# Kernel optimization log

Hardware: AMD Instinct MI355X
Metric: run time of the kernel (lower is better)

Reference implementation:

```python
import jax, jax.numpy as jnp
import numpy as np

R, C, N, E, H, F, ED, G, L = 1, 4, 50000, 200000, 128, 128, 16, 64, 2


def setup_inputs() -> dict:
    key = jax.random.key(0)
    ks = jax.random.split(key, 16)
    s = 0.05
    return {
        "x": jax.random.normal(ks[0], (R * C * N, H), jnp.float32),
        "batch": jnp.sort(jax.random.randint(ks[1], (N,), 0, G)),
        "edge_index": jax.random.randint(ks[2], (2, E), 0, N),
        "edge_attr": jax.random.normal(ks[3], (1, 1, E, ED), jnp.float32),
        "node_mask": jax.random.uniform(ks[4], (R, C, N, 1), jnp.float32),
        "edge_mask": jax.random.uniform(ks[5], (R, C, E, 1), jnp.float32),
        "W_be": jax.random.normal(ks[6], (ED, H), jnp.float32) * s,
        "b_be": jnp.zeros((H,), jnp.float32),
        "eps": jnp.zeros((L,), jnp.float32),
        "W1": jax.random.normal(ks[7], (L, H, H), jnp.float32) * s,
        "b1": jnp.zeros((L, H), jnp.float32),
        "W2": jax.random.normal(ks[8], (L, H, H), jnp.float32) * s,
        "b2": jnp.zeros((L, H), jnp.float32),
        "Wm1": jax.random.normal(ks[9], (H, H), jnp.float32) * s,
        "bm1": jnp.zeros((H,), jnp.float32),
        "Wm2": jax.random.normal(ks[10], (H, F), jnp.float32) * s,
        "bm2": jnp.zeros((F,), jnp.float32),
    }


def reference(x, batch, edge_index, edge_attr, node_mask, edge_mask,
              W_be, b_be, eps, W1, b1, W2, b2, Wm1, bm1, Wm2, bm2):
    gelu = lambda v: jax.nn.gelu(v, approximate=False)  # torch F.gelu default is erf
    src, dst = edge_index[0], edge_index[1]
    # bond encoder, shared across conv layers: (1,1,E,H)
    ee = edge_attr @ W_be + b_be
    for l in range(L):
        ux = x.reshape(R, C, N, H)
        # gather + add + GELU + edge-weight multiply: (R,C,E,H)
        msg = gelu(ux[:, :, src, :] + ee) * edge_mask
        # scatter_sum over edges into destination nodes
        agg = jnp.zeros_like(ux).at[:, :, dst, :].add(msg)
        h = (1.0 + eps[l]) * x + agg.reshape(x.shape)
        # conv MLP: Linear -> GELU -> Linear, then outer GELU (norm=Identity, dropout=0)
        h = gelu(h @ W1[l] + b1[l]) @ W2[l] + b2[l]
        x = gelu(h)
    # final node MLP (PyG MLP, norm=None): Linear -> GELU -> Linear
    x = gelu(x @ Wm1 + bm1) @ Wm2 + bm2  # (R*C*N, F)
    x4 = x.reshape(R, C, N, F)
    # masked mean-pool per (repeat, centroid, graph)
    num = jnp.zeros((R, C, G, F), x.dtype).at[:, :, batch, :].add(x4 * node_mask)
    den = jnp.zeros((R, C, G, 1), x.dtype).at[:, :, batch, :].add(node_mask) + 1e-7
    pooled = (num / den).transpose(0, 2, 1, 3).reshape(-1, F)  # (R*G*C, F)
    return pooled
```

## Files before the change

### kernel.cpp

```cpp
#include <hip/hip_runtime.h>
#include <math.h>

#define NN 50000
#define EN 200000
#define CC 4
#define HH 128
#define GG 64
#define LDSA 136
#define LDSF 132

typedef __attribute__((ext_vector_type(8))) short bs8;
typedef __attribute__((ext_vector_type(4))) float f32x4;

__device__ __forceinline__ unsigned short f2bf(float f) {
  unsigned int u = __float_as_uint(f);
  u += 0x7FFFu + ((u >> 16) & 1u);
  return (unsigned short)(u >> 16);
}
__device__ __forceinline__ float bf2f(unsigned short h) {
  return __uint_as_float(((unsigned int)h) << 16);
}
__device__ __forceinline__ float gelu_f(float x) {
  float z = fabsf(x) * 0.7071067811865476f;
  float t = __builtin_amdgcn_rcpf(fmaf(0.3275911f, z, 1.0f));
  float poly = t * fmaf(t, fmaf(t, fmaf(t, fmaf(t, 1.061405429f, -1.453152027f),
                                        1.421413741f), -0.284496736f), 0.254829592f);
  float e = fmaf(-poly, __expf(-z * z), 1.0f);
  return 0.5f * x * (1.0f + copysignf(e, x));
}
__device__ __forceinline__ float gelu2_f(float x) {
  float z = fabsf(x) * 0.7071067811865476f;
  float t = __builtin_amdgcn_rcpf(fmaf(0.3275911f, z, 1.0f));
  float poly = t * fmaf(t, fmaf(t, fmaf(t, fmaf(t, 1.061405429f, -1.453152027f),
                                        1.421413741f), -0.284496736f), 0.254829592f);
  float e = fmaf(-poly, __expf(-z * z), 1.0f);
  return x * (1.0f + copysignf(e, x));
}

__global__ __launch_bounds__(256) void count_kernel(const int* __restrict__ dst,
                                                    int* __restrict__ counts) {
  int e = blockIdx.x * 256 + threadIdx.x;
  if (e < EN) atomicAdd(&counts[dst[e]], 1);
}

__global__ __launch_bounds__(256) void block_sum_kernel(const int* __restrict__ counts,
                                                        int* __restrict__ bsums) {
  int tid = threadIdx.x;
  int i = blockIdx.x * 256 + tid;
  int v = (i < NN) ? counts[i] : 0;
#pragma unroll
  for (int d = 1; d < 64; d <<= 1) v += __shfl_xor(v, d);
  __shared__ int ws4[4];
  if ((tid & 63) == 0) ws4[tid >> 6] = v;
  __syncthreads();
  if (tid == 0) bsums[blockIdx.x] = ws4[0] + ws4[1] + ws4[2] + ws4[3];
}

__global__ __launch_bounds__(256) void bsum_scan_kernel(const int* __restrict__ bsums,
                                                        int* __restrict__ boffs, int nb) {
  int tid = threadIdx.x, lane = tid & 63, wv = tid >> 6;
  int v = (tid < nb) ? bsums[tid] : 0;
  int s = v;
#pragma unroll
  for (int d = 1; d < 64; d <<= 1) { int t = __shfl_up(s, d); if (lane >= d) s += t; }
  __shared__ int wsum[4];
  if (lane == 63) wsum[wv] = s;
  __syncthreads();
  int pre = 0;
  for (int j = 0; j < wv; ++j) pre += wsum[j];
  if (tid < nb) boffs[tid] = pre + s - v;
}

__global__ __launch_bounds__(256) void block_scan_kernel(const int* __restrict__ counts,
                                                         const int* __restrict__ boffs,
                                                         int* __restrict__ offsets,
                                                         int* __restrict__ cursor) {
  int tid = threadIdx.x, lane = tid & 63, wv = tid >> 6;
  int i = blockIdx.x * 256 + tid;
  int v = (i < NN) ? counts[i] : 0;
  int s = v;
#pragma unroll
  for (int d = 1; d < 64; d <<= 1) { int t = __shfl_up(s, d); if (lane >= d) s += t; }
  __shared__ int wsum[4];
  if (lane == 63) wsum[wv] = s;
  __syncthreads();
  int pre = boffs[blockIdx.x];
  for (int j = 0; j < wv; ++j) pre += wsum[j];
  if (i < NN) { int e = pre + s - v; offsets[i] = e; cursor[i] = e; }
  if (i == 0) offsets[NN] = EN;
}

__global__ __launch_bounds__(256) void fill_kernel(const int* __restrict__ dst,
                                                   int* __restrict__ cursor,
                                                   int* __restrict__ csr_e) {
  int e = blockIdx.x * 256 + threadIdx.x;
  if (e < EN) {
    int pos = atomicAdd(&cursor[dst[e]], 1);
    csr_e[pos] = e;
  }
}

__global__ __launch_bounds__(256) void prep_w_kernel(const float* __restrict__ W1,
                                                     const float* __restrict__ W2,
                                                     const float* __restrict__ Wm1,
                                                     const float* __restrict__ Wm2,
                                                     unsigned short* __restrict__ wts) {
  int m = blockIdx.x >> 6;
  int idx = (blockIdx.x & 63) * 256 + threadIdx.x;
  const float* src = (m == 0) ? W1 : (m == 1) ? W1 + 16384 : (m == 2) ? W2
                     : (m == 3) ? W2 + 16384 : (m == 4) ? Wm1 : Wm2;
  unsigned short* dhi = wts + m * 32768;
  unsigned short* dlo = dhi + 16384;
  int n = idx >> 7, k = idx & 127;
  float v = src[k * HH + n];
  unsigned short hi = f2bf(v);
  dhi[n * HH + k] = hi;
  dlo[n * HH + k] = f2bf(v - bf2f(hi));
}

__global__ __launch_bounds__(256) void ee_kernel(const float* __restrict__ eattr,
                                                 const float* __restrict__ Wbe,
                                                 const float* __restrict__ bbe,
                                                 float* __restrict__ ee) {
  __shared__ float Ws[16 * HH];
  __shared__ float Ea[16 * 16];
  int tid = threadIdx.x;
  int e0 = blockIdx.x * 16;
#pragma unroll
  for (int i = 0; i < 8; ++i) Ws[tid + i * 256] = Wbe[tid + i * 256];
  Ea[tid] = eattr[(size_t)e0 * 16 + tid];
  __syncthreads();
  int h = tid & 127, half = tid >> 7;
  float bb = bbe[h];
#pragma unroll
  for (int j = 0; j < 8; ++j) {
    int el = j * 2 + half;
    float acc = bb;
#pragma unroll
    for (int d = 0; d < 16; ++d) acc += Ea[el * 16 + d] * Ws[d * HH + h];
    ee[(size_t)(e0 + el) * HH + h] = acc;
  }
}

__global__ __launch_bounds__(256) void agg_kernel(const float* __restrict__ x,
                                                  const float* __restrict__ ee,
                                                  const float* __restrict__ emask,
                                                  const int* __restrict__ src,
                                                  const int* __restrict__ off,
                                                  const int* __restrict__ csr_e,
                                                  const float* __restrict__ epsp, int layer,
                                                  float* __restrict__ hout) {
  int wv = threadIdx.x >> 6, lane = threadIdx.x & 63;
  int v = blockIdx.x * 4 + wv;
  int c2 = lane * 2;
  float2 acc[CC];
#pragma unroll
  for (int c = 0; c < CC; ++c) { acc[c].x = 0.f; acc[c].y = 0.f; }
  int beg = off[v], end = off[v + 1];

  float2 eeC; float2 xC[CC]; float emC[CC];
  int eN = 0, sN = 0;
  eeC.x = 0.f; eeC.y = 0.f;
#pragma unroll
  for (int c = 0; c < CC; ++c) { xC[c].x = 0.f; xC[c].y = 0.f; emC[c] = 0.f; }

  if (beg < end) {
    int e0 = csr_e[beg];
    int s0 = src[e0];
    eeC = *(const float2*)(ee + (size_t)e0 * HH + c2);
#pragma unroll
    for (int c = 0; c < CC; ++c) {
      xC[c] = *(const float2*)(x + ((size_t)c * NN + s0) * HH + c2);
      emC[c] = 0.5f * emask[(size_t)c * EN + e0];
    }
    if (beg + 1 < end) { eN = csr_e[beg + 1]; sN = src[eN]; }
  }

  for (int t = beg; t < end; ++t) {
    float2 eeB; float2 xB[CC]; float emB[CC];
    int eNN = 0, sNN = 0;
    if (t + 1 < end) {
      eeB = *(const float2*)(ee + (size_t)eN * HH + c2);
#pragma unroll
      for (int c = 0; c < CC; ++c) {
        xB[c] = *(const float2*)(x + ((size_t)c * NN + sN) * HH + c2);
        emB[c] = 0.5f * emask[(size_t)c * EN + eN];
      }
      if (t + 2 < end) { eNN = csr_e[t + 2]; sNN = src[eNN]; }
    } else {
      eeB.x = 0.f; eeB.y = 0.f;
#pragma unroll
      for (int c = 0; c < CC; ++c) { xB[c].x = 0.f; xB[c].y = 0.f; emB[c] = 0.f; }
    }
#pragma unroll
    for (int c = 0; c < CC; ++c) {
      acc[c].x += gelu2_f(xC[c].x + eeC.x) * emC[c];
      acc[c].y += gelu2_f(xC[c].y + eeC.y) * emC[c];
    }
    eeC = eeB;
#pragma unroll
    for (int c = 0; c < CC; ++c) { xC[c] = xB[c]; emC[c] = emB[c]; }
    eN = eNN; sN = sNN;
  }

  float ep = 1.0f + epsp[layer];
#pragma unroll
  for (int c = 0; c < CC; ++c) {
    float2 xs = *(const float2*)(x + ((size_t)c * NN + v) * HH + c2);
    float2 o;
    o.x = fmaf(ep, xs.x, acc[c].x);
    o.y = fmaf(ep, xs.y, acc[c].y);
    *(float2*)(hout + ((size_t)c * NN + v) * HH + c2) = o;
  }
}

__global__ __launch_bounds__(256, 2) void mlp_kernel(
    const float* __restrict__ in,
    const unsigned short* __restrict__ w1hi, const unsigned short* __restrict__ w1lo,
    const float* __restrict__ b1,
    const unsigned short* __restrict__ w2hi, const unsigned short* __restrict__ w2lo,
    const float* __restrict__ b2,
    float* __restrict__ out) {
  __shared__ __align__(16) unsigned short AB[2 * 64 * HH];
  unsigned short* Ahi = AB;
  unsigned short* Alo = AB + 64 * HH;
  int tid = threadIdx.x;
  int row0 = blockIdx.x * 64;
  int lane = tid & 63, wq = tid >> 6;
  int ln = lane & 15, quad = lane >> 4;

  bs8 b1h[4][2], b1l[4][2];
#pragma unroll
  for (int ks = 0; ks < 4; ++ks)
#pragma unroll
    for (int nt = 0; nt < 2; ++nt) {
      int wrow = ((wq * 2 + nt) * 16 + ln) * HH + ks * 32 + quad * 8;
      b1h[ks][nt] = *(const bs8*)(w1hi + wrow);
      b1l[ks][nt] = *(const bs8*)(w1lo + wrow);
    }

#pragma unroll
  for (int i = 0; i < 4; ++i) {
    int idx = tid + i * 256;
    int r = idx >> 4, blk = idx & 15;
    const float* p = in + (size_t)(row0 + r) * HH + blk * 8;
    float4 v0 = *(const float4*)p;
    float4 v1 = *(const float4*)(p + 4);
    bs8 h, l;
    h[0] = f2bf(v0.x); h[1] = f2bf(v0.y); h[2] = f2bf(v0.z); h[3] = f2bf(v0.w);
    h[4] = f2bf(v1.x); h[5] = f2bf(v1.y); h[6] = f2bf(v1.z); h[7] = f2bf(v1.w);
    l[0] = f2bf(v0.x - bf2f(h[0])); l[1] = f2bf(v0.y - bf2f(h[1]));
    l[2] = f2bf(v0.z - bf2f(h[2])); l[3] = f2bf(v0.w - bf2f(h[3]));
    l[4] = f2bf(v1.x - bf2f(h[4])); l[5] = f2bf(v1.y - bf2f(h[5]));
    l[6] = f2bf(v1.z - bf2f(h[6])); l[7] = f2bf(v1.w - bf2f(h[7]));
    int sb = blk ^ (r & 15);
    *(bs8*)(Ahi + r * HH + sb * 8) = h;
    *(bs8*)(Alo + r * HH + sb * 8) = l;
  }
  __syncthreads();

  f32x4 acc[4][2];
#pragma unroll
  for (int mt = 0; mt < 4; ++mt)
#pragma unroll
    for (int nt = 0; nt < 2; ++nt)
#pragma unroll
      for (int r = 0; r < 4; ++r) acc[mt][nt][r] = 0.f;
#pragma unroll
  for (int ks = 0; ks < 4; ++ks) {
    bs8 ah[4], al[4];
    int sb = ((ks * 4 + quad) ^ ln) * 8;
#pragma unroll
    for (int mt = 0; mt < 4; ++mt) {
      ah[mt] = *(const bs8*)(Ahi + (mt * 16 + ln) * HH + sb);
      al[mt] = *(const bs8*)(Alo + (mt * 16 + ln) * HH + sb);
    }
#pragma unroll
    for (int nt = 0; nt < 2; ++nt)
#pragma unroll
      for (int mt = 0; mt < 4; ++mt) {
        acc[mt][nt] = __builtin_amdgcn_mfma_f32_16x16x32_bf16(al[mt], b1h[ks][nt], acc[mt][nt], 0, 0, 0);
        acc[mt][nt] = __builtin_amdgcn_mfma_f32_16x16x32_bf16(ah[mt], b1l[ks][nt], acc[mt][nt], 0, 0, 0);
        acc[mt][nt] = __builtin_amdgcn_mfma_f32_16x16x32_bf16(ah[mt], b1h[ks][nt], acc[mt][nt], 0, 0, 0);
      }
  }
  __syncthreads();

  bs8 b2h[4][2], b2l[4][2];
#pragma unroll
  for (int ks = 0; ks < 4; ++ks)
#pragma unroll
    for (int nt = 0; nt < 2; ++nt) {
      int wrow = ((wq * 2 + nt) * 16 + ln) * HH + ks * 32 + quad * 8;
      b2h[ks][nt] = *(const bs8*)(w2hi + wrow);
      b2l[ks][nt] = *(const bs8*)(w2lo + wrow);
    }

#pragma unroll
  for (int nt = 0; nt < 2; ++nt) {
    int col = (wq * 2 + nt) * 16 + ln;
    int cb = col >> 3, co = col & 7;
    float bb = b1[col];
#pragma unroll
    for (int mt = 0; mt < 4; ++mt)
#pragma unroll
      for (int r = 0; r < 4; ++r) {
        float tv = gelu_f(acc[mt][nt][r] + bb);
        unsigned short th = f2bf(tv);
        int rr = mt * 16 + quad * 4 + r;
        int sof = rr * HH + (cb ^ (rr & 15)) * 8 + co;
        Ahi[sof] = th;
        Alo[sof] = f2bf(tv - bf2f(th));
      }
  }
  __syncthreads();

#pragma unroll
  for (int mt = 0; mt < 4; ++mt)
#pragma unroll
    for (int nt = 0; nt < 2; ++nt)
#pragma unroll
      for (int r = 0; r < 4; ++r) acc[mt][nt][r] = 0.f;
#pragma unroll
  for (int ks = 0; ks < 4; ++ks) {
    bs8 ah[4], al[4];
    int sb = ((ks * 4 + quad) ^ ln) * 8;
#pragma unroll
    for (int mt = 0; mt < 4; ++mt) {
      ah[mt] = *(const bs8*)(Ahi + (mt * 16 + ln) * HH + sb);
      al[mt] = *(const bs8*)(Alo + (mt * 16 + ln) * HH + sb);
    }
#pragma unroll
    for (int nt = 0; nt < 2; ++nt)
#pragma unroll
      for (int mt = 0; mt < 4; ++mt) {
        acc[mt][nt] = __builtin_amdgcn_mfma_f32_16x16x32_bf16(al[mt], b2h[ks][nt], acc[mt][nt], 0, 0, 0);
        acc[mt][nt] = __builtin_amdgcn_mfma_f32_16x16x32_bf16(ah[mt], b2l[ks][nt], acc[mt][nt], 0, 0, 0);
        acc[mt][nt] = __builtin_amdgcn_mfma_f32_16x16x32_bf16(ah[mt], b2h[ks][nt], acc[mt][nt], 0, 0, 0);
      }
  }
#pragma unroll
  for (int nt = 0; nt < 2; ++nt) {
    int col = (wq * 2 + nt) * 16 + ln;
    float bb = b2[col];
#pragma unroll
    for (int mt = 0; mt < 4; ++mt)
#pragma unroll
      for (int r = 0; r < 4; ++r) {
        float o = gelu_f(acc[mt][nt][r] + bb);
        out[(size_t)(row0 + mt * 16 + quad * 4 + r) * HH + col] = o;
      }
  }
}

__global__ __launch_bounds__(256, 2) void mlp_pool_kernel(
    const float* __restrict__ in,
    const unsigned short* __restrict__ w1hi, const unsigned short* __restrict__ w1lo,
    const float* __restrict__ b1,
    const unsigned short* __restrict__ w2hi, const unsigned short* __restrict__ w2lo,
    const float* __restrict__ b2,
    const float* __restrict__ nmask, const int* __restrict__ batch,
    float* __restrict__ num) {
  __shared__ __align__(16) unsigned short AB[128 * LDSA];
  __shared__ int kk[64];
  unsigned short* Ahi = AB;
  unsigned short* Alo = AB + 64 * LDSA;
  int tid = threadIdx.x;
  int row0 = blockIdx.x * 64;
  int lane = tid & 63, wq = tid >> 6;
  int ln = lane & 15, quad = lane >> 4;

  bs8 b1h[4][2], b1l[4][2];
#pragma unroll
  for (int ks = 0; ks < 4; ++ks)
#pragma unroll
    for (int nt = 0; nt < 2; ++nt) {
      int wrow = ((wq * 2 + nt) * 16 + ln) * HH + ks * 32 + quad * 8;
      b1h[ks][nt] = *(const bs8*)(w1hi + wrow);
      b1l[ks][nt] = *(const bs8*)(w1lo + wrow);
    }
#pragma unroll
  for (int i = 0; i < 8; ++i) {
    int idx = tid + i * 256;
    int r = idx >> 5, cc4 = idx & 31;
    float4 vv = *(const float4*)(in + (size_t)(row0 + r) * HH + cc4 * 4);
    unsigned short h0 = f2bf(vv.x), h1 = f2bf(vv.y), h2 = f2bf(vv.z), h3 = f2bf(vv.w);
    ushort4 hv; hv.x = h0; hv.y = h1; hv.z = h2; hv.w = h3;
    ushort4 lv;
    lv.x = f2bf(vv.x - bf2f(h0)); lv.y = f2bf(vv.y - bf2f(h1));
    lv.z = f2bf(vv.z - bf2f(h2)); lv.w = f2bf(vv.w - bf2f(h3));
    *(ushort4*)(Ahi + r * LDSA + cc4 * 4) = hv;
    *(ushort4*)(Alo + r * LDSA + cc4 * 4) = lv;
  }
  if (tid < 64) {
    int gr = row0 + tid;
    int c = gr / NN;
    int n = gr - c * NN;
    kk[tid] = (c << 6) | batch[n];
  }
  __syncthreads();

  f32x4 acc[4][2];
#pragma unroll
  for (int mt = 0; mt < 4; ++mt)
#pragma unroll
    for (int nt = 0; nt < 2; ++nt)
#pragma unroll
      for (int r = 0; r < 4; ++r) acc[mt][nt][r] = 0.f;
#pragma unroll
  for (int ks = 0; ks < 4; ++ks) {
    bs8 ah[4], al[4];
#pragma unroll
    for (int mt = 0; mt < 4; ++mt) {
      ah[mt] = *(const bs8*)(Ahi + (mt * 16 + ln) * LDSA + ks * 32 + quad * 8);
      al[mt] = *(const bs8*)(Alo + (mt * 16 + ln) * LDSA + ks * 32 + quad * 8);
    }
#pragma unroll
    for (int nt = 0; nt < 2; ++nt)
#pragma unroll
      for (int mt = 0; mt < 4; ++mt) {
        acc[mt][nt] = __builtin_amdgcn_mfma_f32_16x16x32_bf16(al[mt], b1h[ks][nt], acc[mt][nt], 0, 0, 0);
        acc[mt][nt] = __builtin_amdgcn_mfma_f32_16x16x32_bf16(ah[mt], b1l[ks][nt], acc[mt][nt], 0, 0, 0);
        acc[mt][nt] = __builtin_amdgcn_mfma_f32_16x16x32_bf16(ah[mt], b1h[ks][nt], acc[mt][nt], 0, 0, 0);
      }
  }
  __syncthreads();

  bs8 b2h[4][2], b2l[4][2];
#pragma unroll
  for (int ks = 0; ks < 4; ++ks)
#pragma unroll
    for (int nt = 0; nt < 2; ++nt) {
      int wrow = ((wq * 2 + nt) * 16 + ln) * HH + ks * 32 + quad * 8;
      b2h[ks][nt] = *(const bs8*)(w2hi + wrow);
      b2l[ks][nt] = *(const bs8*)(w2lo + wrow);
    }
#pragma unroll
  for (int nt = 0; nt < 2; ++nt) {
    int col = (wq * 2 + nt) * 16 + ln;
    float bb = b1[col];
#pragma unroll
    for (int mt = 0; mt < 4; ++mt)
#pragma unroll
      for (int r = 0; r < 4; ++r) {
        float tv = gelu_f(acc[mt][nt][r] + bb);
        unsigned short th = f2bf(tv);
        int rr = mt * 16 + quad * 4 + r;
        Ahi[rr * LDSA + col] = th;
        Alo[rr * LDSA + col] = f2bf(tv - bf2f(th));
      }
  }
  __syncthreads();

#pragma unroll
  for (int mt = 0; mt < 4; ++mt)
#pragma unroll
    for (int nt = 0; nt < 2; ++nt)
#pragma unroll
      for (int r = 0; r < 4; ++r) acc[mt][nt][r] = 0.f;
#pragma unroll
  for (int ks = 0; ks < 4; ++ks) {
    bs8 ah[4], al[4];
#pragma unroll
    for (int mt = 0; mt < 4; ++mt) {
      ah[mt] = *(const bs8*)(Ahi + (mt * 16 + ln) * LDSA + ks * 32 + quad * 8);
      al[mt] = *(const bs8*)(Alo + (mt * 16 + ln) * LDSA + ks * 32 + quad * 8);
    }
#pragma unroll
    for (int nt = 0; nt < 2; ++nt)
#pragma unroll
      for (int mt = 0; mt < 4; ++mt) {
        acc[mt][nt] = __builtin_amdgcn_mfma_f32_16x16x32_bf16(al[mt], b2h[ks][nt], acc[mt][nt], 0, 0, 0);
        acc[mt][nt] = __builtin_amdgcn_mfma_f32_16x16x32_bf16(ah[mt], b2l[ks][nt], acc[mt][nt], 0, 0, 0);
        acc[mt][nt] = __builtin_amdgcn_mfma_f32_16x16x32_bf16(ah[mt], b2h[ks][nt], acc[mt][nt], 0, 0, 0);
      }
  }
  __syncthreads();
  float* Tf = (float*)AB;
#pragma unroll
  for (int nt = 0; nt < 2; ++nt) {
    int col = (wq * 2 + nt) * 16 + ln;
    float bb = b2[col];
#pragma unroll
    for (int mt = 0; mt < 4; ++mt)
#pragma unroll
      for (int r = 0; r < 4; ++r) {
        int rl = mt * 16 + quad * 4 + r;
        int gr = row0 + rl;
        Tf[rl * LDSF + col] = (acc[mt][nt][r] + bb) * nmask[gr];
      }
  }
  __syncthreads();
  if (tid < 128) {
    int col = tid;
    float a2 = 0.f;
    int cur = kk[0];
    for (int r = 0; r < 64; ++r) {
      int k2 = kk[r];
      if (k2 != cur) {
        atomicAdd(&num[((size_t)(cur & 63) * CC + (cur >> 6)) * HH + col], a2);
        a2 = 0.f;
        cur = k2;
      }
      a2 += Tf[r * LDSF + col];
    }
    atomicAdd(&num[((size_t)(cur & 63) * CC + (cur >> 6)) * HH + col], a2);
  }
}

__global__ __launch_bounds__(256) void pool_finalize_kernel(const float* __restrict__ num,
                                                            const int* __restrict__ batch,
                                                            const float* __restrict__ nmask,
                                                            float* __restrict__ outp) {
  int g = blockIdx.x >> 2, c = blockIdx.x & 3;
  int lo = 0, hi = NN;
  while (lo < hi) { int m = (lo + hi) >> 1; if (batch[m] < g) lo = m + 1; else hi = m; }
  int start = lo;
  hi = NN;
  while (lo < hi) { int m = (lo + hi) >> 1; if (batch[m] < g + 1) lo = m + 1; else hi = m; }
  int end = lo;
  int tid = threadIdx.x;
  float d = 0.f;
  for (int n = start + tid; n < end; n += 256) d += nmask[c * NN + n];
#pragma unroll
  for (int k = 1; k < 64; k <<= 1) d += __shfl_xor(d, k);
  __shared__ float ws4[4];
  if ((tid & 63) == 0) ws4[tid >> 6] = d;
  __syncthreads();
  float den = ws4[0] + ws4[1] + ws4[2] + ws4[3] + 1e-7f;
  if (tid < 128) {
    int idx = blockIdx.x * 128 + tid;
    outp[idx] = num[idx] / den;
  }
}

extern "C" void kernel_launch(void* const* d_in, const int* in_sizes, int n_in,
                              void* d_out, int out_size, void* d_ws, size_t ws_size,
                              hipStream_t stream) {
  const float* x_in  = (const float*)d_in[0];
  const int*   batch = (const int*)d_in[1];
  const int*   eidx  = (const int*)d_in[2];
  const float* eattr = (const float*)d_in[3];
  const float* nmask = (const float*)d_in[4];
  const float* emask = (const float*)d_in[5];
  const float* Wbe   = (const float*)d_in[6];
  const float* bbe   = (const float*)d_in[7];
  const float* epsp  = (const float*)d_in[8];
  const float* W1    = (const float*)d_in[9];
  const float* b1    = (const float*)d_in[10];
  const float* W2    = (const float*)d_in[11];
  const float* b2    = (const float*)d_in[12];
  const float* Wm1   = (const float*)d_in[13];
  const float* bm1   = (const float*)d_in[14];
  const float* Wm2   = (const float*)d_in[15];
  const float* bm2   = (const float*)d_in[16];
  float* outp = (float*)d_out;

  const int* srcp = eidx;
  const int* dstp = eidx + EN;

  char* ws = (char*)d_ws;
  float* ee   = (float*)(ws);
  float* hbuf = (float*)(ws + 102400000);
  float* xbuf = (float*)(ws + 204800000);
  int* counts  = (int*)(ws + 307200000);
  int* offsets = counts + NN;
  int* cursor  = offsets + NN + 1;
  int* csr_e   = cursor + NN;
  unsigned short* wts = (unsigned short*)(ws + 307200000 + 1400016);
  int* bsums = (int*)ws;
  int* boffs = (int*)(ws + 1024);
  float* num = (float*)ws;

  const int NB = (NN + 255) / 256;

  hipMemsetAsync(counts, 0, NN * sizeof(int), stream);
  count_kernel<<<(EN + 255) / 256, 256, 0, stream>>>(dstp, counts);
  block_sum_kernel<<<NB, 256, 0, stream>>>(counts, bsums);
  bsum_scan_kernel<<<1, 256, 0, stream>>>(bsums, boffs, NB);
  block_scan_kernel<<<NB, 256, 0, stream>>>(counts, boffs, offsets, cursor);
  fill_kernel<<<(EN + 255) / 256, 256, 0, stream>>>(dstp, cursor, csr_e);

  prep_w_kernel<<<384, 256, 0, stream>>>(W1, W2, Wm1, Wm2, wts);

  ee_kernel<<<EN / 16, 256, 0, stream>>>(eattr, Wbe, bbe, ee);

  agg_kernel<<<NN / 4, 256, 0, stream>>>(x_in, ee, emask, srcp, offsets, csr_e, epsp, 0, hbuf);
  mlp_kernel<<<(CC * NN) / 64, 256, 0, stream>>>(hbuf, wts + 0, wts + 16384, b1,
                                                 wts + 65536, wts + 81920, b2, xbuf);
  agg_kernel<<<NN / 4, 256, 0, stream>>>(xbuf, ee, emask, srcp, offsets, csr_e, epsp, 1, hbuf);
  mlp_kernel<<<(CC * NN) / 64, 256, 0, stream>>>(hbuf, wts + 32768, wts + 49152, b1 + 128,
                                                 wts + 98304, wts + 114688, b2 + 128, xbuf);
  hipMemsetAsync(num, 0, 131072, stream);
  mlp_pool_kernel<<<(CC * NN) / 64, 256, 0, stream>>>(xbuf, wts + 131072, wts + 147456, bm1,
                                                      wts + 163840, wts + 180224, bm2,
                                                      nmask, batch, num);
  pool_finalize_kernel<<<GG * CC, 256, 0, stream>>>(num, batch, nmask, outp);
}
```

Baseline: 714.1 us.

## Pack edge src and masks into CSR order; use nontemporal streaming loads/stores

The CSR fill kernel now writes each edge's id and source index together, plus its four per-centroid edge masks as a float4, in destination-sorted order. The aggregation kernel then reads these contiguously instead of chasing csr_e→src and making four scattered emask loads per edge. The h buffer is now written with nontemporal stores and read back in the MLP kernels with nontemporal loads, to reduce cache pollution. The cost is a larger fill kernel and extra workspace for the packed arrays.

```diff
diff --git a/kernel.cpp b/kernel.cpp
--- a/kernel.cpp
+++ b/kernel.cpp
@@ -11,6 +11,7 @@
 
 typedef __attribute__((ext_vector_type(8))) short bs8;
 typedef __attribute__((ext_vector_type(4))) float f32x4;
+typedef __attribute__((ext_vector_type(2))) float f32x2;
 
 __device__ __forceinline__ unsigned short f2bf(float f) {
   unsigned int u = __float_as_uint(f);
@@ -91,12 +92,21 @@
 }
 
 __global__ __launch_bounds__(256) void fill_kernel(const int* __restrict__ dst,
+                                                   const int* __restrict__ src,
+                                                   const float* __restrict__ emask,
                                                    int* __restrict__ cursor,
-                                                   int* __restrict__ csr_e) {
+                                                   int2* __restrict__ csr_es,
+                                                   float4* __restrict__ emask_s) {
   int e = blockIdx.x * 256 + threadIdx.x;
   if (e < EN) {
+    int s = src[e];
+    float m0 = emask[e];
+    float m1 = emask[EN + e];
+    float m2 = emask[2 * EN + e];
+    float m3 = emask[3 * EN + e];
     int pos = atomicAdd(&cursor[dst[e]], 1);
-    csr_e[pos] = e;
+    csr_es[pos] = make_int2(e, s);
+    emask_s[pos] = make_float4(m0, m1, m2, m3);
   }
 }
 
@@ -144,10 +154,9 @@
 
 __global__ __launch_bounds__(256) void agg_kernel(const float* __restrict__ x,
                                                   const float* __restrict__ ee,
-                                                  const float* __restrict__ emask,
-                                                  const int* __restrict__ src,
                                                   const int* __restrict__ off,
-                                                  const int* __restrict__ csr_e,
+                                                  const int2* __restrict__ csr_es,
+                                                  const float4* __restrict__ emask_s,
                                                   const float* __restrict__ epsp, int layer,
                                                   float* __restrict__ hout) {
   int wv = threadIdx.x >> 6, lane = threadIdx.x & 63;
@@ -159,34 +168,33 @@
   int beg = off[v], end = off[v + 1];
 
   float2 eeC; float2 xC[CC]; float emC[CC];
-  int eN = 0, sN = 0;
+  int2 esN = make_int2(0, 0);
   eeC.x = 0.f; eeC.y = 0.f;
 #pragma unroll
   for (int c = 0; c < CC; ++c) { xC[c].x = 0.f; xC[c].y = 0.f; emC[c] = 0.f; }
 
   if (beg < end) {
-    int e0 = csr_e[beg];
-    int s0 = src[e0];
-    eeC = *(const float2*)(ee + (size_t)e0 * HH + c2);
-#pragma unroll
-    for (int c = 0; c < CC; ++c) {
-      xC[c] = *(const float2*)(x + ((size_t)c * NN + s0) * HH + c2);
-      emC[c] = 0.5f * emask[(size_t)c * EN + e0];
-    }
-    if (beg + 1 < end) { eN = csr_e[beg + 1]; sN = src[eN]; }
+    int2 es0 = csr_es[beg];
+    eeC = *(const float2*)(ee + (size_t)es0.x * HH + c2);
+#pragma unroll
+    for (int c = 0; c < CC; ++c)
+      xC[c] = *(const float2*)(x + ((size_t)c * NN + es0.y) * HH + c2);
+    float4 m = emask_s[beg];
+    emC[0] = 0.5f * m.x; emC[1] = 0.5f * m.y; emC[2] = 0.5f * m.z; emC[3] = 0.5f * m.w;
+    if (beg + 1 < end) esN = csr_es[beg + 1];
   }
 
   for (int t = beg; t < end; ++t) {
     float2 eeB; float2 xB[CC]; float emB[CC];
-    int eNN = 0, sNN = 0;
+    int2 esNN = make_int2(0, 0);
     if (t + 1 < end) {
-      eeB = *(const float2*)(ee + (size_t)eN * HH + c2);
-#pragma unroll
-      for (int c = 0; c < CC; ++c) {
-        xB[c] = *(const float2*)(x + ((size_t)c * NN + sN) * HH + c2);
-        emB[c] = 0.5f * emask[(size_t)c * EN + eN];
-      }
-      if (t + 2 < end) { eNN = csr_e[t + 2]; sNN = src[eNN]; }
+      eeB = *(const float2*)(ee + (size_t)esN.x * HH + c2);
+#pragma unroll
+      for (int c = 0; c < CC; ++c)
+        xB[c] = *(const float2*)(x + ((size_t)c * NN + esN.y) * HH + c2);
+      float4 m = emask_s[t + 1];
+      emB[0] = 0.5f * m.x; emB[1] = 0.5f * m.y; emB[2] = 0.5f * m.z; emB[3] = 0.5f * m.w;
+      if (t + 2 < end) esNN = csr_es[t + 2];
     } else {
       eeB.x = 0.f; eeB.y = 0.f;
 #pragma unroll
@@ -200,17 +208,17 @@
     eeC = eeB;
 #pragma unroll
     for (int c = 0; c < CC; ++c) { xC[c] = xB[c]; emC[c] = emB[c]; }
-    eN = eNN; sN = sNN;
+    esN = esNN;
   }
 
   float ep = 1.0f + epsp[layer];
 #pragma unroll
   for (int c = 0; c < CC; ++c) {
     float2 xs = *(const float2*)(x + ((size_t)c * NN + v) * HH + c2);
-    float2 o;
-    o.x = fmaf(ep, xs.x, acc[c].x);
-    o.y = fmaf(ep, xs.y, acc[c].y);
-    *(float2*)(hout + ((size_t)c * NN + v) * HH + c2) = o;
+    f32x2 o;
+    o[0] = fmaf(ep, xs.x, acc[c].x);
+    o[1] = fmaf(ep, xs.y, acc[c].y);
+    __builtin_nontemporal_store(o, (f32x2*)(hout + ((size_t)c * NN + v) * HH + c2));
   }
 }
 
@@ -244,15 +252,15 @@
     int idx = tid + i * 256;
     int r = idx >> 4, blk = idx & 15;
     const float* p = in + (size_t)(row0 + r) * HH + blk * 8;
-    float4 v0 = *(const float4*)p;
-    float4 v1 = *(const float4*)(p + 4);
+    f32x4 v0 = __builtin_nontemporal_load((const f32x4*)p);
+    f32x4 v1 = __builtin_nontemporal_load((const f32x4*)(p + 4));
     bs8 h, l;
-    h[0] = f2bf(v0.x); h[1] = f2bf(v0.y); h[2] = f2bf(v0.z); h[3] = f2bf(v0.w);
-    h[4] = f2bf(v1.x); h[5] = f2bf(v1.y); h[6] = f2bf(v1.z); h[7] = f2bf(v1.w);
-    l[0] = f2bf(v0.x - bf2f(h[0])); l[1] = f2bf(v0.y - bf2f(h[1]));
-    l[2] = f2bf(v0.z - bf2f(h[2])); l[3] = f2bf(v0.w - bf2f(h[3]));
-    l[4] = f2bf(v1.x - bf2f(h[4])); l[5] = f2bf(v1.y - bf2f(h[5]));
-    l[6] = f2bf(v1.z - bf2f(h[6])); l[7] = f2bf(v1.w - bf2f(h[7]));
+    h[0] = f2bf(v0[0]); h[1] = f2bf(v0[1]); h[2] = f2bf(v0[2]); h[3] = f2bf(v0[3]);
+    h[4] = f2bf(v1[0]); h[5] = f2bf(v1[1]); h[6] = f2bf(v1[2]); h[7] = f2bf(v1[3]);
+    l[0] = f2bf(v0[0] - bf2f(h[0])); l[1] = f2bf(v0[1] - bf2f(h[1]));
+    l[2] = f2bf(v0[2] - bf2f(h[2])); l[3] = f2bf(v0[3] - bf2f(h[3]));
+    l[4] = f2bf(v1[0] - bf2f(h[4])); l[5] = f2bf(v1[1] - bf2f(h[5]));
+    l[6] = f2bf(v1[2] - bf2f(h[6])); l[7] = f2bf(v1[3] - bf2f(h[7]));
     int sb = blk ^ (r & 15);
     *(bs8*)(Ahi + r * HH + sb * 8) = h;
     *(bs8*)(Alo + r * HH + sb * 8) = l;
@@ -383,12 +391,13 @@
   for (int i = 0; i < 8; ++i) {
     int idx = tid + i * 256;
     int r = idx >> 5, cc4 = idx & 31;
-    float4 vv = *(const float4*)(in + (size_t)(row0 + r) * HH + cc4 * 4);
-    unsigned short h0 = f2bf(vv.x), h1 = f2bf(vv.y), h2 = f2bf(vv.z), h3 = f2bf(vv.w);
+    f32x4 vv = __builtin_nontemporal_load(
+        (const f32x4*)(in + (size_t)(row0 + r) * HH + cc4 * 4));
+    unsigned short h0 = f2bf(vv[0]), h1 = f2bf(vv[1]), h2 = f2bf(vv[2]), h3 = f2bf(vv[3]);
     ushort4 hv; hv.x = h0; hv.y = h1; hv.z = h2; hv.w = h3;
     ushort4 lv;
-    lv.x = f2bf(vv.x - bf2f(h0)); lv.y = f2bf(vv.y - bf2f(h1));
-    lv.z = f2bf(vv.z - bf2f(h2)); lv.w = f2bf(vv.w - bf2f(h3));
+    lv.x = f2bf(vv[0] - bf2f(h0)); lv.y = f2bf(vv[1] - bf2f(h1));
+    lv.z = f2bf(vv[2] - bf2f(h2)); lv.w = f2bf(vv[3] - bf2f(h3));
     *(ushort4*)(Ahi + r * LDSA + cc4 * 4) = hv;
     *(ushort4*)(Alo + r * LDSA + cc4 * 4) = lv;
   }
@@ -564,10 +573,11 @@
   float* hbuf = (float*)(ws + 102400000);
   float* xbuf = (float*)(ws + 204800000);
   int* counts  = (int*)(ws + 307200000);
-  int* offsets = counts + NN;
-  int* cursor  = offsets + NN + 1;
-  int* csr_e   = cursor + NN;
-  unsigned short* wts = (unsigned short*)(ws + 307200000 + 1400016);
+  int* offsets = (int*)(ws + 307400000);
+  int* cursor  = (int*)(ws + 307600008);
+  int2* csr_es = (int2*)(ws + 307800016);
+  float4* emask_s = (float4*)(ws + 309400016);
+  unsigned short* wts = (unsigned short*)(ws + 312600016);
   int* bsums = (int*)ws;
   int* boffs = (int*)(ws + 1024);
   float* num = (float*)ws;
@@ -579,16 +589,16 @@
   block_sum_kernel<<<NB, 256, 0, stream>>>(counts, bsums);
   bsum_scan_kernel<<<1, 256, 0, stream>>>(bsums, boffs, NB);
   block_scan_kernel<<<NB, 256, 0, stream>>>(counts, boffs, offsets, cursor);
-  fill_kernel<<<(EN + 255) / 256, 256, 0, stream>>>(dstp, cursor, csr_e);
+  fill_kernel<<<(EN + 255) / 256, 256, 0, stream>>>(dstp, srcp, emask, cursor, csr_es, emask_s);
 
   prep_w_kernel<<<384, 256, 0, stream>>>(W1, W2, Wm1, Wm2, wts);
 
   ee_kernel<<<EN / 16, 256, 0, stream>>>(eattr, Wbe, bbe, ee);
 
-  agg_kernel<<<NN / 4, 256, 0, stream>>>(x_in, ee, emask, srcp, offsets, csr_e, epsp, 0, hbuf);
+  agg_kernel<<<NN / 4, 256, 0, stream>>>(x_in, ee, offsets, csr_es, emask_s, epsp, 0, hbuf);
   mlp_kernel<<<(CC * NN) / 64, 256, 0, stream>>>(hbuf, wts + 0, wts + 16384, b1,
                                                  wts + 65536, wts + 81920, b2, xbuf);
-  agg_kernel<<<NN / 4, 256, 0, stream>>>(xbuf, ee, emask, srcp, offsets, csr_e, epsp, 1, hbuf);
+  agg_kernel<<<NN / 4, 256, 0, stream>>>(xbuf, ee, offsets, csr_es, emask_s, epsp, 1, hbuf);
   mlp_kernel<<<(CC * NN) / 64, 256, 0, stream>>>(hbuf, wts + 32768, wts + 49152, b1 + 128,
                                                  wts + 98304, wts + 114688, b2 + 128, xbuf);
   hipMemsetAsync(num, 0, 131072, stream);
```

Measured after the change: 717.2 us. About the same (+0.4%).
